# Performance work log

Measured on AMD Instinct MI355X. Metric: run time of the kernel, lower is better.

The kernel has to match this reference:

```python
import jax, jax.numpy as jnp
import numpy as np

N_TYPES = 4  # global / and / or / leaf node types (indep_weights)


def gcn_layer(x, W_stack, b, edge_src, edge_dst, edge_w, labels, num_nodes):
    # Per-node-type dense projection: compute all 4 projections, then select by label.
    # all4: [4, N, out]
    all4 = jnp.einsum('nd,kdo->kno', x, W_stack)
    support = jnp.take_along_axis(all4, labels[None, :, None].astype(jnp.int32), axis=0)[0]  # [N, out]
    # Sparse adjacency propagation: out[dst] += w * support[src]  (torch.spmm equivalent)
    msgs = support[edge_src] * edge_w[:, None]  # [E, out]
    agg = jax.ops.segment_sum(msgs, edge_dst, num_segments=num_nodes)
    return agg + b


def setup_inputs() -> dict:
    key = jax.random.key(0)
    ks = jax.random.split(key, 12)
    N, E = 50000, 1600000
    nfeat, nhid, nclass = 256, 256, 64
    x = jax.random.normal(ks[0], (N, nfeat), dtype=jnp.float32)
    edge_src = jax.random.randint(ks[1], (E,), 0, N, dtype=jnp.int32)
    edge_dst = jax.random.randint(ks[2], (E,), 0, N, dtype=jnp.int32)
    edge_w = jax.random.uniform(ks[3], (E,), dtype=jnp.float32)
    labels = jax.random.randint(ks[4], (N,), 0, N_TYPES, dtype=jnp.int32)
    def winit(k, fi, fo):
        s = 1.0 / np.sqrt(fo)
        return jax.random.uniform(k, (N_TYPES, fi, fo), minval=-s, maxval=s, dtype=jnp.float32)
    def binit(k, fo):
        s = 1.0 / np.sqrt(fo)
        return jax.random.uniform(k, (fo,), minval=-s, maxval=s, dtype=jnp.float32)
    return {
        'x': x, 'edge_src': edge_src, 'edge_dst': edge_dst, 'edge_w': edge_w, 'labels': labels,
        'W1': winit(ks[5], nfeat, nhid), 'b1': binit(ks[6], nhid),
        'W2': winit(ks[7], nhid, nhid), 'b2': binit(ks[8], nhid),
        'W3': winit(ks[9], nhid, nclass), 'b3': binit(ks[10], nclass),
    }


def reference(x, edge_src, edge_dst, edge_w, labels, W1, b1, W2, b2, W3, b3):
    N = x.shape[0]
    h = jax.nn.relu(gcn_layer(x, W1, b1, edge_src, edge_dst, edge_w, labels, N))
    # F.dropout with p=0 (module default) is identity
    h = jax.nn.relu(gcn_layer(h, W2, b2, edge_src, edge_dst, edge_w, labels, N))
    out = gcn_layer(h, W3, b3, edge_src, edge_dst, edge_w, labels, N)
    return out
```

## Files before the change

### kernel.cpp

```cpp
#include <hip/hip_runtime.h>
#include <hip/hip_bf16.h>

#define NT 4
#define FEAT 256
#define OUT3 64

typedef __bf16 bf16x8 __attribute__((ext_vector_type(8)));
typedef float  f32x4  __attribute__((ext_vector_type(4)));

__device__ inline unsigned int f2bf_bits(float f) {
    __hip_bfloat16 h = __float2bfloat16(f);
    unsigned short u;
    __builtin_memcpy(&u, &h, 2);
    return (unsigned int)u;
}
__device__ inline float bfl(unsigned int u) { return __uint_as_float(u << 16); }
__device__ inline float bfh(unsigned int u) { return __uint_as_float(u & 0xffff0000u); }
__device__ __host__ inline int nat_of(int p) {
    int lo = p & 63;
    return (p & ~63) | (((lo & 3) << 4) | (lo >> 2));
}

__global__ __launch_bounds__(512) void pass_a(const int* __restrict__ dst,
                                              const int* __restrict__ labels,
                                              int* __restrict__ bcnt, int* __restrict__ lc,
                                              int E, int N) {
    __shared__ int h[256];
    __shared__ int lh[NT];
    int tid = threadIdx.x;
    if (tid < 256) h[tid] = 0;
    if (tid < NT) lh[tid] = 0;
    __syncthreads();
    int base = blockIdx.x * 4096;
#pragma unroll
    for (int k = 0; k < 8; ++k) {
        int e = base + k * 512 + tid;
        if (e < E) atomicAdd(&h[((unsigned)dst[e]) >> 8], 1);
    }
#pragma unroll
    for (int k = 0; k < 8; ++k) {
        int i = base + k * 512 + tid;
        if (i < N) atomicAdd(&lh[labels[i]], 1);
    }
    __syncthreads();
    if (tid < 256) { int v = h[tid]; if (v) atomicAdd(&bcnt[tid], v); }
    if (tid < NT) { int v = lh[tid]; if (v) atomicAdd(&lc[tid], v); }
}

__global__ __launch_bounds__(256) void scan_master(
    const int* __restrict__ bcnt, const int* __restrict__ lc,
    int* __restrict__ boff, int* __restrict__ gcur, int* __restrict__ rowoff,
    int* __restrict__ lstart, int NB, int N, int E) {
    __shared__ int s[256];
    int tid = threadIdx.x;
    int own = (tid < NB) ? bcnt[tid] : 0;
    s[tid] = own;
    __syncthreads();
    for (int d = 1; d < 256; d <<= 1) {
        int v = (tid >= d) ? s[tid - d] : 0;
        __syncthreads();
        s[tid] += v;
        __syncthreads();
    }
    int excl = s[tid] - own;
    if (tid < NB) { boff[tid] = excl; gcur[tid] = excl; }
    if (tid == 0) {
        boff[NB] = E; rowoff[N] = E;
        int run = 0;
        for (int l = 0; l < NT; ++l) {
            lstart[l] = run;
            run += (lc[l] + 63) & ~63;
        }
    }
}

__global__ void scatter_nodes(const int* __restrict__ labels, const int* __restrict__ lstart,
                              int* __restrict__ lcur, int* __restrict__ iperm, int N) {
    int n = blockIdx.x * 256 + threadIdx.x;
    int lab = (n < N) ? labels[n] : -1;
    int lane = threadIdx.x & 63;
    for (int l = 0; l < NT; ++l) {
        unsigned long long m = __ballot(lab == l);
        if (m == 0ull) continue;
        int leader = __builtin_ctzll(m);
        int base = 0;
        if (lane == leader) base = atomicAdd(&lcur[l], (int)__popcll(m));
        base = __shfl(base, leader, 64);
        if (lab == l) {
            int prefix = (int)__popcll(m & ((1ull << lane) - 1ull));
            iperm[n] = lstart[l] + base + prefix;
        }
    }
}

__global__ __launch_bounds__(512) void fuse_a(
    const int* __restrict__ src, const int* __restrict__ dst, const float* __restrict__ w,
    const int* __restrict__ iperm, int* __restrict__ gcur, uint2* __restrict__ earr, int E,
    const float* __restrict__ x, unsigned short* __restrict__ actLo,
    unsigned short* __restrict__ actHi, int total4,
    const float* __restrict__ W1, const float* __restrict__ W2, const float* __restrict__ W3,
    const float* __restrict__ b1, const float* __restrict__ b2,
    unsigned short* __restrict__ W1b, unsigned short* __restrict__ W2b,
    unsigned short* __restrict__ W3b, float* __restrict__ biasPerm,
    int nbEB, int nbX) {
    int tid = threadIdx.x;
    int blk = (int)blockIdx.x;
    if (blk < nbEB) {
        __shared__ int h[256];
        __shared__ int basearr[256];
        if (tid < 256) h[tid] = 0;
        __syncthreads();
        int base = blk * 4096;
        int b[8], rank[8], px[8]; float wv[8];
#pragma unroll
        for (int k = 0; k < 8; ++k) {
            int e = base + k * 512 + tid;
            if (e < E) {
                int d = dst[e];
                b[k] = ((unsigned)d) >> 8;
                px[k] = iperm[src[e]] | ((d & 255) << 16);
                wv[k] = w[e];
                rank[k] = atomicAdd(&h[b[k]], 1);
            } else b[k] = -1;
        }
        __syncthreads();
        if (tid < 256) { int c = h[tid]; basearr[tid] = c ? atomicAdd(&gcur[tid], c) : 0; }
        __syncthreads();
#pragma unroll
        for (int k = 0; k < 8; ++k) {
            if (b[k] >= 0) {
                int pos = basearr[b[k]] + rank[k];
                earr[pos] = make_uint2((unsigned)px[k], __float_as_uint(wv[k]));
            }
        }
    } else if (blk < nbEB + nbX) {
        int i = (blk - nbEB) * 512 + tid;
        if (i < total4) {
            float4 v = ((const float4*)x)[i];
            unsigned int lo = f2bf_bits(v.x) | (f2bf_bits(v.y) << 16);
            unsigned int hi = f2bf_bits(v.z) | (f2bf_bits(v.w) << 16);
            int slot = iperm[i >> 6];
            unsigned short* dp = ((i & 63) >= 32) ? actHi : actLo;
            ((uint2*)dp)[(size_t)slot * 32 + (i & 31)] = make_uint2(lo, hi);
        }
    } else {
        const int S = NT * FEAT * FEAT;
        const int S3 = NT * FEAT * OUT3;
        int idx = (blk - nbEB - nbX) * 512 + tid;
        if (idx < 2 * S + S3) {
            const float* W; unsigned short* D; int OUTF; int t; bool remap;
            if (idx < S)          { W = W1; D = W1b; OUTF = FEAT; t = idx;         remap = false; }
            else if (idx < 2 * S) { W = W2; D = W2b; OUTF = FEAT; t = idx - S;     remap = true; }
            else                  { W = W3; D = W3b; OUTF = OUT3; t = idx - 2 * S; remap = true; }
            int n = t % OUTF;
            int r = t / OUTF;
            int j = r & 7, q = (r >> 3) & 3, k0 = (r >> 5) & 7, lab = r >> 8;
            int k_slot = k0 * 32 + q * 8 + j;
            int k_src = remap ? nat_of(k_slot) : k_slot;
            float f = W[((size_t)(lab * FEAT + k_src)) * OUTF + n];
            D[(((size_t)lab * 8 + k0) * OUTF + n) * 32 + q * 8 + j] = (unsigned short)f2bf_bits(f);
        } else {
            int p2 = idx - (2 * S + S3);
            if (p2 < 256) biasPerm[p2] = b1[nat_of(p2)];
            else if (p2 < 512) biasPerm[p2] = b2[nat_of(p2 - 256)];
        }
    }
}

__device__ void bucket_sort_body(int b, const uint2* __restrict__ earr,
                                 const int* __restrict__ boff, int* __restrict__ rowoff,
                                 unsigned int* __restrict__ edata, int N) {
    int s = boff[b], e = boff[b + 1];
    __shared__ int cnt[256], off[256];
    int tid = threadIdx.x;
    cnt[tid] = 0;
    __syncthreads();
    for (int i = s + tid; i < e; i += 256) atomicAdd(&cnt[(earr[i].x >> 16) & 255], 1);
    __syncthreads();
    off[tid] = cnt[tid];
    __syncthreads();
    for (int d = 1; d < 256; d <<= 1) {
        int v = (tid >= d) ? off[tid - d] : 0;
        __syncthreads();
        off[tid] += v;
        __syncthreads();
    }
    int excl = off[tid] - cnt[tid];
    int node = b * 256 + tid;
    if (node < N) rowoff[node] = s + excl;
    off[tid] = excl;
    __syncthreads();
    for (int i = s + tid; i < e; i += 256) {
        uint2 r = earr[i];
        int d = (r.x >> 16) & 255;
        int k = atomicAdd(&off[d], 1);
        edata[s + k] = (f2bf_bits(__uint_as_float(r.y)) << 16) | (r.x & 0xffff);
    }
}

__device__ void proj256_body(int gb,
                             const unsigned short* __restrict__ actLo,
                             const unsigned short* __restrict__ actHi,
                             const unsigned short* __restrict__ Wswz,
                             const int* __restrict__ lstart,
                             unsigned short* __restrict__ supLo,
                             unsigned short* __restrict__ supHi) {
    int warp = threadIdx.x >> 6;
    int lane = threadIdx.x & 63;
    int m0 = gb * 64;
    int lab = (m0 >= lstart[1]) + (m0 >= lstart[2]) + (m0 >= lstart[3]);
    int q = lane >> 4, c = lane & 15;
    int n0 = warp * 64;

    const unsigned short* aLo = actLo + (size_t)(m0 + c) * 128 + q * 8;
    const unsigned short* aHi = actHi + (size_t)(m0 + c) * 128 + q * 8;
    const unsigned short* bb = Wswz + (size_t)lab * FEAT * 256 + (size_t)(n0 + c) * 32 + q * 8;

    f32x4 acc[4][4] = {};
#pragma unroll
    for (int k0 = 0; k0 < 8; ++k0) {
        const unsigned short* abase = (k0 < 4) ? aLo : aHi;
        int koff = (k0 & 3) * 32;
        bf16x8 a[4];
#pragma unroll
        for (int t = 0; t < 4; ++t) a[t] = *(const bf16x8*)(abase + (size_t)t * 2048 + koff);
        const unsigned short* bk = bb + (size_t)k0 * 32 * 256;
#pragma unroll
        for (int u = 0; u < 4; ++u) {
            bf16x8 bfrag = *(const bf16x8*)(bk + u * 512);
#pragma unroll
            for (int t = 0; t < 4; ++t)
                acc[t][u] = __builtin_amdgcn_mfma_f32_16x16x32_bf16(a[t], bfrag, acc[t][u], 0, 0, 0);
        }
    }
    uint2* ov = (uint2*)((n0 >= 128) ? supHi : supLo);
    int cix = ((n0 & 64) >> 2) + c;
#pragma unroll
    for (int t = 0; t < 4; ++t) {
#pragma unroll
        for (int r = 0; r < 4; ++r) {
            int row = m0 + t * 16 + q * 4 + r;
            unsigned int lo = f2bf_bits(acc[t][0][r]) | (f2bf_bits(acc[t][1][r]) << 16);
            unsigned int hi = f2bf_bits(acc[t][2][r]) | (f2bf_bits(acc[t][3][r]) << 16);
            ov[(size_t)row * 32 + cix] = make_uint2(lo, hi);
        }
    }
}

__global__ __launch_bounds__(256) void fuse_b(
    const uint2* __restrict__ earr, const int* __restrict__ boff,
    int* __restrict__ rowoff, unsigned int* __restrict__ edata, int N, int NB,
    const unsigned short* __restrict__ actLo, const unsigned short* __restrict__ actHi,
    const unsigned short* __restrict__ Wswz, const int* __restrict__ lstart,
    unsigned short* __restrict__ supLo, unsigned short* __restrict__ supHi) {
    int blk = (int)blockIdx.x;
    if (blk < NB) bucket_sort_body(blk, earr, boff, rowoff, edata, N);
    else proj256_body(blk - NB, actLo, actHi, Wswz, lstart, supLo, supHi);
}

__global__ __launch_bounds__(256) void proj256_kernel(
    const unsigned short* __restrict__ actLo, const unsigned short* __restrict__ actHi,
    const unsigned short* __restrict__ Wswz, const int* __restrict__ lstart,
    unsigned short* __restrict__ supLo, unsigned short* __restrict__ supHi) {
    proj256_body((int)blockIdx.x, actLo, actHi, Wswz, lstart, supLo, supHi);
}

__global__ __launch_bounds__(256) void proj64_kernel(
    const unsigned short* __restrict__ actLo, const unsigned short* __restrict__ actHi,
    const unsigned short* __restrict__ Wswz, const int* __restrict__ lstart,
    unsigned short* __restrict__ outp) {
    int warp = threadIdx.x >> 6;
    int lane = threadIdx.x & 63;
    int m0 = blockIdx.x * 64;
    int lab = (m0 >= lstart[1]) + (m0 >= lstart[2]) + (m0 >= lstart[3]);
    int q = lane >> 4, c = lane & 15;
    int mb = m0 + warp * 16;

    const unsigned short* aLo = actLo + (size_t)(mb + c) * 128 + q * 8;
    const unsigned short* aHi = actHi + (size_t)(mb + c) * 128 + q * 8;
    const unsigned short* bb = Wswz + (size_t)lab * FEAT * OUT3 + (size_t)c * 32 + q * 8;

    f32x4 acc[4] = {};
#pragma unroll
    for (int k0 = 0; k0 < 8; ++k0) {
        const unsigned short* abase = (k0 < 4) ? aLo : aHi;
        bf16x8 a = *(const bf16x8*)(abase + (k0 & 3) * 32);
        const unsigned short* bk = bb + (size_t)k0 * 32 * OUT3;
#pragma unroll
        for (int u = 0; u < 4; ++u) {
            bf16x8 bfrag = *(const bf16x8*)(bk + u * 512);
            acc[u] = __builtin_amdgcn_mfma_f32_16x16x32_bf16(a, bfrag, acc[u], 0, 0, 0);
        }
    }
    uint2* ov = (uint2*)outp;
#pragma unroll
    for (int r = 0; r < 4; ++r) {
        int row = mb + q * 4 + r;
        unsigned int lo = f2bf_bits(acc[0][r]) | (f2bf_bits(acc[1][r]) << 16);
        unsigned int hi = f2bf_bits(acc[2][r]) | (f2bf_bits(acc[3][r]) << 16);
        ov[(size_t)row * 16 + c] = make_uint2(lo, hi);
    }
}

__global__ __launch_bounds__(256) void agg256h_kernel(
    const unsigned int* __restrict__ sup, const int* __restrict__ rowoff,
    const unsigned int* __restrict__ edata, const int* __restrict__ iperm,
    const float* __restrict__ biasHalf, unsigned int* __restrict__ outp, int N) {
    int warp = __builtin_amdgcn_readfirstlane((int)(threadIdx.x >> 6));
    int node = (int)blockIdx.x * 4 + warp;
    if (node >= N) return;
    int lane = threadIdx.x & 63;
    int s = __builtin_amdgcn_readfirstlane(rowoff[node]);
    int e = __builtin_amdgcn_readfirstlane(rowoff[node + 1]);
    int slot = __builtin_amdgcn_readfirstlane(iperm[node]);
    float a0 = 0.f, a1 = 0.f;
    int j = s;
    for (; j + 16 <= e; j += 16) {
        unsigned int ed[16], v[16];
#pragma unroll
        for (int u = 0; u < 16; ++u) ed[u] = edata[j + u];
        __builtin_amdgcn_sched_barrier(0);
#pragma unroll
        for (int u = 0; u < 16; ++u) v[u] = sup[(size_t)(ed[u] & 0xffff) * 64 + lane];
        __builtin_amdgcn_sched_barrier(0);
#pragma unroll
        for (int u = 0; u < 16; ++u) {
            float w = __uint_as_float(ed[u] & 0xffff0000u);
            a0 += w * bfl(v[u]); a1 += w * bfh(v[u]);
        }
    }
    if (j < e) {
        unsigned int ed[16], v[16]; float wm[16];
#pragma unroll
        for (int u = 0; u < 16; ++u) {
            int jj = j + u;
            int jc = (jj < e) ? jj : e - 1;
            ed[u] = edata[jc];
            wm[u] = (jj < e) ? __uint_as_float(ed[u] & 0xffff0000u) : 0.f;
        }
        __builtin_amdgcn_sched_barrier(0);
#pragma unroll
        for (int u = 0; u < 16; ++u) v[u] = sup[(size_t)(ed[u] & 0xffff) * 64 + lane];
        __builtin_amdgcn_sched_barrier(0);
#pragma unroll
        for (int u = 0; u < 16; ++u) { a0 += wm[u] * bfl(v[u]); a1 += wm[u] * bfh(v[u]); }
    }
    float2 b = ((const float2*)biasHalf)[lane];
    a0 = fmaxf(a0 + b.x, 0.f);
    a1 = fmaxf(a1 + b.y, 0.f);
    unsigned int o = f2bf_bits(a0) | (f2bf_bits(a1) << 16);
    __builtin_nontemporal_store(o, &outp[(size_t)slot * 64 + lane]);
}

__global__ __launch_bounds__(256) void agg64_kernel(
    const unsigned short* __restrict__ sup, const int* __restrict__ rowoff,
    const unsigned int* __restrict__ edata, const float* __restrict__ b3,
    float* __restrict__ outp, int N) {
    int warp = __builtin_amdgcn_readfirstlane((int)(threadIdx.x >> 6));
    int node = (int)blockIdx.x * 4 + warp;
    if (node >= N) return;
    int lane = threadIdx.x & 63;
    int s = __builtin_amdgcn_readfirstlane(rowoff[node]);
    int e = __builtin_amdgcn_readfirstlane(rowoff[node + 1]);
    float a = 0.f;
    int j = s;
    for (; j + 16 <= e; j += 16) {
        unsigned int ed[16]; unsigned short v[16];
#pragma unroll
        for (int u = 0; u < 16; ++u) ed[u] = edata[j + u];
        __builtin_amdgcn_sched_barrier(0);
#pragma unroll
        for (int u = 0; u < 16; ++u) v[u] = sup[(size_t)(ed[u] & 0xffff) * 64 + lane];
        __builtin_amdgcn_sched_barrier(0);
#pragma unroll
        for (int u = 0; u < 16; ++u)
            a += __uint_as_float(ed[u] & 0xffff0000u) * __uint_as_float((unsigned int)v[u] << 16);
    }
    if (j < e) {
        unsigned int ed[16]; float wm[16]; unsigned short v[16];
#pragma unroll
        for (int u = 0; u < 16; ++u) {
            int jj = j + u;
            int jc = (jj < e) ? jj : e - 1;
            ed[u] = edata[jc];
            wm[u] = (jj < e) ? __uint_as_float(ed[u] & 0xffff0000u) : 0.f;
        }
        __builtin_amdgcn_sched_barrier(0);
#pragma unroll
        for (int u = 0; u < 16; ++u) v[u] = sup[(size_t)(ed[u] & 0xffff) * 64 + lane];
        __builtin_amdgcn_sched_barrier(0);
#pragma unroll
        for (int u = 0; u < 16; ++u)
            a += wm[u] * __uint_as_float((unsigned int)v[u] << 16);
    }
    int natp = (((lane & 3) << 4) | (lane >> 2));
    outp[(size_t)node * 64 + natp] = a + b3[natp];
}

extern "C" void kernel_launch(void* const* d_in, const int* in_sizes, int n_in,
                              void* d_out, int out_size, void* d_ws, size_t ws_size,
                              hipStream_t stream) {
    const float* x        = (const float*)d_in[0];
    const int*   edge_src = (const int*)d_in[1];
    const int*   edge_dst = (const int*)d_in[2];
    const float* edge_w   = (const float*)d_in[3];
    const int*   labels   = (const int*)d_in[4];
    const float* W1 = (const float*)d_in[5];
    const float* b1 = (const float*)d_in[6];
    const float* W2 = (const float*)d_in[7];
    const float* b2 = (const float*)d_in[8];
    const float* W3 = (const float*)d_in[9];
    const float* b3 = (const float*)d_in[10];

    const int N = in_sizes[0] / FEAT;
    const int E = in_sizes[1];
    const int NB = (N + 255) >> 8;
    const int G64 = (N + NT * 64 + 63) / 64;
    const int slotCap = G64 * 64;

    char* p = (char*)d_ws;
    auto alloc = [&](size_t bytes) -> char* {
        char* r = p;
        p += (bytes + 255) & ~(size_t)255;
        return r;
    };
    unsigned short* bufA = (unsigned short*)alloc((size_t)slotCap * FEAT * 2);
    unsigned short* bufB = (unsigned short*)alloc((size_t)slotCap * FEAT * 2);
    unsigned short* W1b  = (unsigned short*)alloc((size_t)NT * FEAT * FEAT * 2);
    unsigned short* W2b  = (unsigned short*)alloc((size_t)NT * FEAT * FEAT * 2);
    unsigned short* W3b  = (unsigned short*)alloc((size_t)NT * FEAT * OUT3 * 2);
    float*        biasPerm = (float*)alloc(512 * 4);
    int*          rowoff = (int*)alloc((size_t)(N + 1) * 4);
    unsigned int* edata  = (unsigned int*)alloc((size_t)E * 4);
    int*          iperm  = (int*)alloc((size_t)N * 4);
    int*          counters = (int*)alloc(264 * 4);
    int*          boff   = (int*)alloc(257 * 4);
    int*          gcur   = (int*)alloc(256 * 4);
    int*          lstart = (int*)alloc(64);
    int* bcnt = counters;
    int* lc   = counters + 256;
    int* lcur = counters + 260;

    unsigned short* actLo = bufA;
    unsigned short* actHi = bufA + (size_t)slotCap * 128;
    unsigned short* supLo = bufB;
    unsigned short* supHi = bufB + (size_t)slotCap * 128;
    uint2* earr = (uint2*)d_out;

    const int nbEB = (E + 4095) / 4096;
    const int total4 = N * 64;
    const int nbX = (total4 + 511) / 512;
    const int totW = 2 * NT * FEAT * FEAT + NT * FEAT * OUT3 + 512;
    const int nbW = (totW + 511) / 512;

    hipMemsetAsync(counters, 0, 264 * 4, stream);
    pass_a<<<nbEB, 512, 0, stream>>>(edge_dst, labels, bcnt, lc, E, N);
    scan_master<<<1, 256, 0, stream>>>(bcnt, lc, boff, gcur, rowoff, lstart, NB, N, E);
    scatter_nodes<<<(N + 255) / 256, 256, 0, stream>>>(labels, lstart, lcur, iperm, N);
    fuse_a<<<nbEB + nbX + nbW, 512, 0, stream>>>(
        edge_src, edge_dst, edge_w, iperm, gcur, earr, E,
        x, actLo, actHi, total4,
        W1, W2, W3, b1, b2, W1b, W2b, W3b, biasPerm, nbEB, nbX);

    const int aggGrid = (N + 3) / 4;
    fuse_b<<<NB + G64, 256, 0, stream>>>(earr, boff, rowoff, edata, N, NB,
                                         actLo, actHi, W1b, lstart, supLo, supHi);
    agg256h_kernel<<<aggGrid, 256, 0, stream>>>((const unsigned int*)supLo, rowoff, edata, iperm,
                                                biasPerm + 0, (unsigned int*)actLo, N);
    agg256h_kernel<<<aggGrid, 256, 0, stream>>>((const unsigned int*)supHi, rowoff, edata, iperm,
                                                biasPerm + 128, (unsigned int*)actHi, N);
    proj256_kernel<<<G64, 256, 0, stream>>>(actLo, actHi, W2b, lstart, supLo, supHi);
    agg256h_kernel<<<aggGrid, 256, 0, stream>>>((const unsigned int*)supLo, rowoff, edata, iperm,
                                                biasPerm + 256, (unsigned int*)actLo, N);
    agg256h_kernel<<<aggGrid, 256, 0, stream>>>((const unsigned int*)supHi, rowoff, edata, iperm,
                                                biasPerm + 384, (unsigned int*)actHi, N);
    proj64_kernel<<<G64, 256, 0, stream>>>(actLo, actHi, W3b, lstart, bufB);
    agg64_kernel<<<aggGrid, 256, 0, stream>>>(bufB, rowoff, edata, b3, (float*)d_out, N);
}
```

Measured before the change: 482.2 us.

## Sort CSR rows by source and process 13 nodes per wave in slices

Each CSR row's edges are insertion-sorted by source index after the bucket scatter, so gathers in a row visit increasing addresses. The 256-wide aggregation now gives each wave 13 nodes and walks their edge lists in four interleaved quarter slices, so neighbouring nodes' gathers overlap in time and may share cache lines. The agg64 kernel also loses its scheduling barriers. The costs are a serial insertion sort in the preprocessing kernel, 26 float accumulators per lane, and load imbalance between waves holding high-degree and low-degree nodes.

```diff
diff --git a/kernel.cpp b/kernel.cpp
--- a/kernel.cpp
+++ b/kernel.cpp
@@ -4,6 +4,8 @@
 #define NT 4
 #define FEAT 256
 #define OUT3 64
+#define NPW 13
+#define NS 4
 
 typedef __bf16 bf16x8 __attribute__((ext_vector_type(8)));
 typedef float  f32x4  __attribute__((ext_vector_type(4)));
@@ -188,6 +190,7 @@
     int excl = off[tid] - cnt[tid];
     int node = b * 256 + tid;
     if (node < N) rowoff[node] = s + excl;
+    int rs = s + excl;
     off[tid] = excl;
     __syncthreads();
     for (int i = s + tid; i < e; i += 256) {
@@ -195,6 +198,15 @@
         int d = (r.x >> 16) & 255;
         int k = atomicAdd(&off[d], 1);
         edata[s + k] = (f2bf_bits(__uint_as_float(r.y)) << 16) | (r.x & 0xffff);
+    }
+    __syncthreads();
+    int re = s + off[tid];
+    for (int i = rs + 1; i < re; ++i) {
+        unsigned int key = edata[i];
+        unsigned int ks = key & 0xffffu;
+        int k = i - 1;
+        while (k >= rs && (edata[k] & 0xffffu) > ks) { edata[k + 1] = edata[k]; --k; }
+        edata[k + 1] = key;
     }
 }
 
@@ -302,54 +314,68 @@
     }
 }
 
-__global__ __launch_bounds__(256) void agg256h_kernel(
+__global__ __launch_bounds__(256, 4) void agg256hp_kernel(
     const unsigned int* __restrict__ sup, const int* __restrict__ rowoff,
     const unsigned int* __restrict__ edata, const int* __restrict__ iperm,
     const float* __restrict__ biasHalf, unsigned int* __restrict__ outp, int N) {
-    int warp = __builtin_amdgcn_readfirstlane((int)(threadIdx.x >> 6));
-    int node = (int)blockIdx.x * 4 + warp;
-    if (node >= N) return;
+    int wid = (int)blockIdx.x * 4 + (int)(threadIdx.x >> 6);
     int lane = threadIdx.x & 63;
-    int s = __builtin_amdgcn_readfirstlane(rowoff[node]);
-    int e = __builtin_amdgcn_readfirstlane(rowoff[node + 1]);
-    int slot = __builtin_amdgcn_readfirstlane(iperm[node]);
-    float a0 = 0.f, a1 = 0.f;
-    int j = s;
-    for (; j + 16 <= e; j += 16) {
-        unsigned int ed[16], v[16];
-#pragma unroll
-        for (int u = 0; u < 16; ++u) ed[u] = edata[j + u];
-        __builtin_amdgcn_sched_barrier(0);
-#pragma unroll
-        for (int u = 0; u < 16; ++u) v[u] = sup[(size_t)(ed[u] & 0xffff) * 64 + lane];
-        __builtin_amdgcn_sched_barrier(0);
-#pragma unroll
-        for (int u = 0; u < 16; ++u) {
-            float w = __uint_as_float(ed[u] & 0xffff0000u);
-            a0 += w * bfl(v[u]); a1 += w * bfh(v[u]);
-        }
-    }
-    if (j < e) {
-        unsigned int ed[16], v[16]; float wm[16];
-#pragma unroll
-        for (int u = 0; u < 16; ++u) {
-            int jj = j + u;
-            int jc = (jj < e) ? jj : e - 1;
-            ed[u] = edata[jc];
-            wm[u] = (jj < e) ? __uint_as_float(ed[u] & 0xffff0000u) : 0.f;
-        }
-        __builtin_amdgcn_sched_barrier(0);
-#pragma unroll
-        for (int u = 0; u < 16; ++u) v[u] = sup[(size_t)(ed[u] & 0xffff) * 64 + lane];
-        __builtin_amdgcn_sched_barrier(0);
-#pragma unroll
-        for (int u = 0; u < 16; ++u) { a0 += wm[u] * bfl(v[u]); a1 += wm[u] * bfh(v[u]); }
+    int n0 = wid * NPW;
+    if (n0 >= N) return;
+    int base[NPW], len[NPW];
+    float a0[NPW], a1[NPW];
+#pragma unroll
+    for (int t = 0; t < NPW; ++t) {
+        int n = n0 + t;
+        int s = (n < N) ? __builtin_amdgcn_readfirstlane(rowoff[n]) : 0;
+        int e = (n < N) ? __builtin_amdgcn_readfirstlane(rowoff[n + 1]) : 0;
+        base[t] = s; len[t] = e - s;
+        a0[t] = 0.f; a1[t] = 0.f;
+    }
+#pragma unroll
+    for (int sl = 0; sl < NS; ++sl) {
+#pragma unroll
+        for (int t = 0; t < NPW; ++t) {
+            int j  = base[t] + ((len[t] * sl) >> 2);
+            int j1 = base[t] + ((len[t] * (sl + 1)) >> 2);
+            float aa0 = a0[t], aa1 = a1[t];
+            for (; j + 4 <= j1; j += 4) {
+                unsigned int e0 = edata[j],     e1 = edata[j + 1];
+                unsigned int e2 = edata[j + 2], e3 = edata[j + 3];
+                unsigned int v0 = sup[(size_t)(e0 & 0xffff) * 64 + lane];
+                unsigned int v1 = sup[(size_t)(e1 & 0xffff) * 64 + lane];
+                unsigned int v2 = sup[(size_t)(e2 & 0xffff) * 64 + lane];
+                unsigned int v3 = sup[(size_t)(e3 & 0xffff) * 64 + lane];
+                float w0 = __uint_as_float(e0 & 0xffff0000u);
+                float w1 = __uint_as_float(e1 & 0xffff0000u);
+                float w2 = __uint_as_float(e2 & 0xffff0000u);
+                float w3 = __uint_as_float(e3 & 0xffff0000u);
+                aa0 += w0 * bfl(v0); aa1 += w0 * bfh(v0);
+                aa0 += w1 * bfl(v1); aa1 += w1 * bfh(v1);
+                aa0 += w2 * bfl(v2); aa1 += w2 * bfh(v2);
+                aa0 += w3 * bfl(v3); aa1 += w3 * bfh(v3);
+            }
+            for (; j < j1; ++j) {
+                unsigned int ed = edata[j];
+                unsigned int v = sup[(size_t)(ed & 0xffff) * 64 + lane];
+                float w = __uint_as_float(ed & 0xffff0000u);
+                aa0 += w * bfl(v); aa1 += w * bfh(v);
+            }
+            a0[t] = aa0; a1[t] = aa1;
+        }
     }
     float2 b = ((const float2*)biasHalf)[lane];
-    a0 = fmaxf(a0 + b.x, 0.f);
-    a1 = fmaxf(a1 + b.y, 0.f);
-    unsigned int o = f2bf_bits(a0) | (f2bf_bits(a1) << 16);
-    __builtin_nontemporal_store(o, &outp[(size_t)slot * 64 + lane]);
+#pragma unroll
+    for (int t = 0; t < NPW; ++t) {
+        int n = n0 + t;
+        if (n < N) {
+            int slot = __builtin_amdgcn_readfirstlane(iperm[n]);
+            float r0 = fmaxf(a0[t] + b.x, 0.f);
+            float r1 = fmaxf(a1[t] + b.y, 0.f);
+            unsigned int o = f2bf_bits(r0) | (f2bf_bits(r1) << 16);
+            __builtin_nontemporal_store(o, &outp[(size_t)slot * 64 + lane]);
+        }
+    }
 }
 
 __global__ __launch_bounds__(256) void agg64_kernel(
@@ -368,10 +394,8 @@
         unsigned int ed[16]; unsigned short v[16];
 #pragma unroll
         for (int u = 0; u < 16; ++u) ed[u] = edata[j + u];
-        __builtin_amdgcn_sched_barrier(0);
 #pragma unroll
         for (int u = 0; u < 16; ++u) v[u] = sup[(size_t)(ed[u] & 0xffff) * 64 + lane];
-        __builtin_amdgcn_sched_barrier(0);
 #pragma unroll
         for (int u = 0; u < 16; ++u)
             a += __uint_as_float(ed[u] & 0xffff0000u) * __uint_as_float((unsigned int)v[u] << 16);
@@ -385,10 +409,8 @@
             ed[u] = edata[jc];
             wm[u] = (jj < e) ? __uint_as_float(ed[u] & 0xffff0000u) : 0.f;
         }
-        __builtin_amdgcn_sched_barrier(0);
 #pragma unroll
         for (int u = 0; u < 16; ++u) v[u] = sup[(size_t)(ed[u] & 0xffff) * 64 + lane];
-        __builtin_amdgcn_sched_barrier(0);
 #pragma unroll
         for (int u = 0; u < 16; ++u)
             a += wm[u] * __uint_as_float((unsigned int)v[u] << 16);
@@ -462,18 +484,19 @@
         x, actLo, actHi, total4,
         W1, W2, W3, b1, b2, W1b, W2b, W3b, biasPerm, nbEB, nbX);
 
+    const int gridP = (N + 4 * NPW - 1) / (4 * NPW);
     const int aggGrid = (N + 3) / 4;
     fuse_b<<<NB + G64, 256, 0, stream>>>(earr, boff, rowoff, edata, N, NB,
                                          actLo, actHi, W1b, lstart, supLo, supHi);
-    agg256h_kernel<<<aggGrid, 256, 0, stream>>>((const unsigned int*)supLo, rowoff, edata, iperm,
-                                                biasPerm + 0, (unsigned int*)actLo, N);
-    agg256h_kernel<<<aggGrid, 256, 0, stream>>>((const unsigned int*)supHi, rowoff, edata, iperm,
-                                                biasPerm + 128, (unsigned int*)actHi, N);
+    agg256hp_kernel<<<gridP, 256, 0, stream>>>((const unsigned int*)supLo, rowoff, edata, iperm,
+                                               biasPerm + 0, (unsigned int*)actLo, N);
+    agg256hp_kernel<<<gridP, 256, 0, stream>>>((const unsigned int*)supHi, rowoff, edata, iperm,
+                                               biasPerm + 128, (unsigned int*)actHi, N);
     proj256_kernel<<<G64, 256, 0, stream>>>(actLo, actHi, W2b, lstart, supLo, supHi);
-    agg256h_kernel<<<aggGrid, 256, 0, stream>>>((const unsigned int*)supLo, rowoff, edata, iperm,
-                                                biasPerm + 256, (unsigned int*)actLo, N);
-    agg256h_kernel<<<aggGrid, 256, 0, stream>>>((const unsigned int*)supHi, rowoff, edata, iperm,
-                                                biasPerm + 384, (unsigned int*)actHi, N);
+    agg256hp_kernel<<<gridP, 256, 0, stream>>>((const unsigned int*)supLo, rowoff, edata, iperm,
+                                               biasPerm + 256, (unsigned int*)actLo, N);
+    agg256hp_kernel<<<gridP, 256, 0, stream>>>((const unsigned int*)supHi, rowoff, edata, iperm,
+                                               biasPerm + 384, (unsigned int*)actHi, N);
     proj64_kernel<<<G64, 256, 0, stream>>>(actLo, actHi, W3b, lstart, bufB);
     agg64_kernel<<<aggGrid, 256, 0, stream>>>(bufB, rowoff, edata, b3, (float*)d_out, N);
 }
```

Result: slower. 967.9 us (+100.7%).

## Sub-sort edges by source range and interleave lo/hi aggregation halves

Applied to the files above, without the earlier changes.

The bucket sort now orders each node's incoming edges by the top 3 bits of the source index (2048 shared counters per bucket) and records 8 sub-row offsets per node. Gathers over the support matrix then walk sources in a more ordered pattern, aiming for better cache locality. The two half-width aggregation launches per layer are merged into one interleaved launch, so neighbouring blocks process the lo and hi halves of the same nodes and share the edge list reads. The agg64 sched_barriers are removed. The cost is a larger row-offset array and more shared memory and scan work in the sort.

```diff
diff --git a/kernel.cpp b/kernel.cpp
--- a/kernel.cpp
+++ b/kernel.cpp
@@ -49,7 +49,7 @@
 
 __global__ __launch_bounds__(256) void scan_master(
     const int* __restrict__ bcnt, const int* __restrict__ lc,
-    int* __restrict__ boff, int* __restrict__ gcur, int* __restrict__ rowoff,
+    int* __restrict__ boff, int* __restrict__ gcur, int* __restrict__ rb,
     int* __restrict__ lstart, int NB, int N, int E) {
     __shared__ int s[256];
     int tid = threadIdx.x;
@@ -65,7 +65,7 @@
     int excl = s[tid] - own;
     if (tid < NB) { boff[tid] = excl; gcur[tid] = excl; }
     if (tid == 0) {
-        boff[NB] = E; rowoff[N] = E;
+        boff[NB] = E; rb[(size_t)N * 8] = E;
         int run = 0;
         for (int l = 0; l < NT; ++l) {
             lstart[l] = run;
@@ -168,33 +168,48 @@
 }
 
 __device__ void bucket_sort_body(int b, const uint2* __restrict__ earr,
-                                 const int* __restrict__ boff, int* __restrict__ rowoff,
+                                 const int* __restrict__ boff, int* __restrict__ rb,
                                  unsigned int* __restrict__ edata, int N) {
     int s = boff[b], e = boff[b + 1];
-    __shared__ int cnt[256], off[256];
+    __shared__ int cnt[2048], off[2048], ts[256];
     int tid = threadIdx.x;
-    cnt[tid] = 0;
-    __syncthreads();
-    for (int i = s + tid; i < e; i += 256) atomicAdd(&cnt[(earr[i].x >> 16) & 255], 1);
-    __syncthreads();
-    off[tid] = cnt[tid];
-    __syncthreads();
+#pragma unroll
+    for (int k = 0; k < 8; ++k) cnt[tid * 8 + k] = 0;
+    __syncthreads();
+    for (int i = s + tid; i < e; i += 256) {
+        unsigned int xx = earr[i].x;
+        int key = (((xx >> 16) & 255) << 3) | ((xx & 0xffffu) >> 13);
+        atomicAdd(&cnt[key], 1);
+    }
+    __syncthreads();
+    int run = 0;
+#pragma unroll
+    for (int k = 0; k < 8; ++k) { off[tid * 8 + k] = run; run += cnt[tid * 8 + k]; }
+    ts[tid] = run;
+    __syncthreads();
+    int own = ts[tid];
     for (int d = 1; d < 256; d <<= 1) {
-        int v = (tid >= d) ? off[tid - d] : 0;
-        __syncthreads();
-        off[tid] += v;
-        __syncthreads();
-    }
-    int excl = off[tid] - cnt[tid];
+        int v = (tid >= d) ? ts[tid - d] : 0;
+        __syncthreads();
+        ts[tid] += v;
+        __syncthreads();
+    }
+    int texcl = ts[tid] - own;
+#pragma unroll
+    for (int k = 0; k < 8; ++k) off[tid * 8 + k] += texcl;
+    __syncthreads();
     int node = b * 256 + tid;
-    if (node < N) rowoff[node] = s + excl;
-    off[tid] = excl;
+    if (node < N) {
+#pragma unroll
+        for (int k = 0; k < 8; ++k) rb[(size_t)node * 8 + k] = s + off[tid * 8 + k];
+    }
     __syncthreads();
     for (int i = s + tid; i < e; i += 256) {
         uint2 r = earr[i];
-        int d = (r.x >> 16) & 255;
-        int k = atomicAdd(&off[d], 1);
-        edata[s + k] = (f2bf_bits(__uint_as_float(r.y)) << 16) | (r.x & 0xffff);
+        unsigned int xx = r.x;
+        int key = (((xx >> 16) & 255) << 3) | ((xx & 0xffffu) >> 13);
+        int k = atomicAdd(&off[key], 1);
+        edata[s + k] = (f2bf_bits(__uint_as_float(r.y)) << 16) | (xx & 0xffffu);
     }
 }
 
@@ -249,12 +264,12 @@
 
 __global__ __launch_bounds__(256) void fuse_b(
     const uint2* __restrict__ earr, const int* __restrict__ boff,
-    int* __restrict__ rowoff, unsigned int* __restrict__ edata, int N, int NB,
+    int* __restrict__ rb, unsigned int* __restrict__ edata, int N, int NB,
     const unsigned short* __restrict__ actLo, const unsigned short* __restrict__ actHi,
     const unsigned short* __restrict__ Wswz, const int* __restrict__ lstart,
     unsigned short* __restrict__ supLo, unsigned short* __restrict__ supHi) {
     int blk = (int)blockIdx.x;
-    if (blk < NB) bucket_sort_body(blk, earr, boff, rowoff, edata, N);
+    if (blk < NB) bucket_sort_body(blk, earr, boff, rb, edata, N);
     else proj256_body(blk - NB, actLo, actHi, Wswz, lstart, supLo, supHi);
 }
 
@@ -302,16 +317,21 @@
     }
 }
 
-__global__ __launch_bounds__(256) void agg256h_kernel(
-    const unsigned int* __restrict__ sup, const int* __restrict__ rowoff,
-    const unsigned int* __restrict__ edata, const int* __restrict__ iperm,
-    const float* __restrict__ biasHalf, unsigned int* __restrict__ outp, int N) {
+__global__ __launch_bounds__(256) void agg256x_kernel(
+    const unsigned int* __restrict__ supLo, const unsigned int* __restrict__ supHi,
+    const int* __restrict__ rb, const unsigned int* __restrict__ edata,
+    const int* __restrict__ iperm, const float* __restrict__ biasPerm, int bOff,
+    unsigned int* __restrict__ outLo, unsigned int* __restrict__ outHi, int N) {
+    int blk = (int)blockIdx.x;
+    int half = blk & 1;
     int warp = __builtin_amdgcn_readfirstlane((int)(threadIdx.x >> 6));
-    int node = (int)blockIdx.x * 4 + warp;
+    int node = (blk >> 1) * 4 + warp;
     if (node >= N) return;
     int lane = threadIdx.x & 63;
-    int s = __builtin_amdgcn_readfirstlane(rowoff[node]);
-    int e = __builtin_amdgcn_readfirstlane(rowoff[node + 1]);
+    const unsigned int* sup = half ? supHi : supLo;
+    unsigned int* outp = half ? outHi : outLo;
+    int s = __builtin_amdgcn_readfirstlane(rb[(size_t)node * 8]);
+    int e = __builtin_amdgcn_readfirstlane(rb[(size_t)node * 8 + 8]);
     int slot = __builtin_amdgcn_readfirstlane(iperm[node]);
     float a0 = 0.f, a1 = 0.f;
     int j = s;
@@ -345,7 +365,7 @@
 #pragma unroll
         for (int u = 0; u < 16; ++u) { a0 += wm[u] * bfl(v[u]); a1 += wm[u] * bfh(v[u]); }
     }
-    float2 b = ((const float2*)biasHalf)[lane];
+    float2 b = ((const float2*)(biasPerm + bOff + half * 128))[lane];
     a0 = fmaxf(a0 + b.x, 0.f);
     a1 = fmaxf(a1 + b.y, 0.f);
     unsigned int o = f2bf_bits(a0) | (f2bf_bits(a1) << 16);
@@ -353,25 +373,23 @@
 }
 
 __global__ __launch_bounds__(256) void agg64_kernel(
-    const unsigned short* __restrict__ sup, const int* __restrict__ rowoff,
+    const unsigned short* __restrict__ sup, const int* __restrict__ rb,
     const unsigned int* __restrict__ edata, const float* __restrict__ b3,
     float* __restrict__ outp, int N) {
     int warp = __builtin_amdgcn_readfirstlane((int)(threadIdx.x >> 6));
     int node = (int)blockIdx.x * 4 + warp;
     if (node >= N) return;
     int lane = threadIdx.x & 63;
-    int s = __builtin_amdgcn_readfirstlane(rowoff[node]);
-    int e = __builtin_amdgcn_readfirstlane(rowoff[node + 1]);
+    int s = __builtin_amdgcn_readfirstlane(rb[(size_t)node * 8]);
+    int e = __builtin_amdgcn_readfirstlane(rb[(size_t)node * 8 + 8]);
     float a = 0.f;
     int j = s;
     for (; j + 16 <= e; j += 16) {
         unsigned int ed[16]; unsigned short v[16];
 #pragma unroll
         for (int u = 0; u < 16; ++u) ed[u] = edata[j + u];
-        __builtin_amdgcn_sched_barrier(0);
 #pragma unroll
         for (int u = 0; u < 16; ++u) v[u] = sup[(size_t)(ed[u] & 0xffff) * 64 + lane];
-        __builtin_amdgcn_sched_barrier(0);
 #pragma unroll
         for (int u = 0; u < 16; ++u)
             a += __uint_as_float(ed[u] & 0xffff0000u) * __uint_as_float((unsigned int)v[u] << 16);
@@ -385,10 +403,8 @@
             ed[u] = edata[jc];
             wm[u] = (jj < e) ? __uint_as_float(ed[u] & 0xffff0000u) : 0.f;
         }
-        __builtin_amdgcn_sched_barrier(0);
 #pragma unroll
         for (int u = 0; u < 16; ++u) v[u] = sup[(size_t)(ed[u] & 0xffff) * 64 + lane];
-        __builtin_amdgcn_sched_barrier(0);
 #pragma unroll
         for (int u = 0; u < 16; ++u)
             a += wm[u] * __uint_as_float((unsigned int)v[u] << 16);
@@ -430,7 +446,7 @@
     unsigned short* W2b  = (unsigned short*)alloc((size_t)NT * FEAT * FEAT * 2);
     unsigned short* W3b  = (unsigned short*)alloc((size_t)NT * FEAT * OUT3 * 2);
     float*        biasPerm = (float*)alloc(512 * 4);
-    int*          rowoff = (int*)alloc((size_t)(N + 1) * 4);
+    int*          rb     = (int*)alloc(((size_t)N * 8 + 8) * 4);
     unsigned int* edata  = (unsigned int*)alloc((size_t)E * 4);
     int*          iperm  = (int*)alloc((size_t)N * 4);
     int*          counters = (int*)alloc(264 * 4);
@@ -455,7 +471,7 @@
 
     hipMemsetAsync(counters, 0, 264 * 4, stream);
     pass_a<<<nbEB, 512, 0, stream>>>(edge_dst, labels, bcnt, lc, E, N);
-    scan_master<<<1, 256, 0, stream>>>(bcnt, lc, boff, gcur, rowoff, lstart, NB, N, E);
+    scan_master<<<1, 256, 0, stream>>>(bcnt, lc, boff, gcur, rb, lstart, NB, N, E);
     scatter_nodes<<<(N + 255) / 256, 256, 0, stream>>>(labels, lstart, lcur, iperm, N);
     fuse_a<<<nbEB + nbX + nbW, 512, 0, stream>>>(
         edge_src, edge_dst, edge_w, iperm, gcur, earr, E,
@@ -463,17 +479,15 @@
         W1, W2, W3, b1, b2, W1b, W2b, W3b, biasPerm, nbEB, nbX);
 
     const int aggGrid = (N + 3) / 4;
-    fuse_b<<<NB + G64, 256, 0, stream>>>(earr, boff, rowoff, edata, N, NB,
+    fuse_b<<<NB + G64, 256, 0, stream>>>(earr, boff, rb, edata, N, NB,
                                          actLo, actHi, W1b, lstart, supLo, supHi);
-    agg256h_kernel<<<aggGrid, 256, 0, stream>>>((const unsigned int*)supLo, rowoff, edata, iperm,
-                                                biasPerm + 0, (unsigned int*)actLo, N);
-    agg256h_kernel<<<aggGrid, 256, 0, stream>>>((const unsigned int*)supHi, rowoff, edata, iperm,
-                                                biasPerm + 128, (unsigned int*)actHi, N);
+    agg256x_kernel<<<2 * aggGrid, 256, 0, stream>>>(
+        (const unsigned int*)supLo, (const unsigned int*)supHi, rb, edata, iperm,
+        biasPerm, 0, (unsigned int*)actLo, (unsigned int*)actHi, N);
     proj256_kernel<<<G64, 256, 0, stream>>>(actLo, actHi, W2b, lstart, supLo, supHi);
-    agg256h_kernel<<<aggGrid, 256, 0, stream>>>((const unsigned int*)supLo, rowoff, edata, iperm,
-                                                biasPerm + 256, (unsigned int*)actLo, N);
-    agg256h_kernel<<<aggGrid, 256, 0, stream>>>((const unsigned int*)supHi, rowoff, edata, iperm,
-                                                biasPerm + 384, (unsigned int*)actHi, N);
+    agg256x_kernel<<<2 * aggGrid, 256, 0, stream>>>(
+        (const unsigned int*)supLo, (const unsigned int*)supHi, rb, edata, iperm,
+        biasPerm, 256, (unsigned int*)actLo, (unsigned int*)actHi, N);
     proj64_kernel<<<G64, 256, 0, stream>>>(actLo, actHi, W3b, lstart, bufB);
-    agg64_kernel<<<aggGrid, 256, 0, stream>>>(bufB, rowoff, edata, b3, (float*)d_out, N);
-}
+    agg64_kernel<<<aggGrid, 256, 0, stream>>>(bufB, rb, edata, b3, (float*)d_out, N);
+}
```

Result: no change. 475.0 us, median of 2 (-1.5%).
